# Kernel tuning notes

Hardware: AMD Instinct MI355X
Metric: run time of the kernel (lower is better)

## Reference

```python
import jax, jax.numpy as jnp
import numpy as np

# CCN 'Contract18': the 18 permutation-equivariant ways to reduce a 3rd-order
# vertex-pair tensor T[i,j,k,c] to a 2nd-order tensor out[a,b,c], with
# summations restricted to the neighborhood via the adjacency matrix A.
#  - 6 single-index sums (choose summed index x placement of the two free ones)
#  - 6 diagonal extractions (two indices tied, 3 pairs x 2 placements)
#  - 6 double sums -> vector, broadcast along rows or columns
# Sums over an index m are weighted by A[a, m] (restrict to neighbors of the
# output row node a); diagonal extractions are unweighted.

N = 256
C = 16

def setup_inputs() -> dict:
    key = jax.random.key(0)
    k1, k2 = jax.random.split(key)
    activations = jax.random.normal(k1, (N, N, N, C), dtype=jnp.float32)
    # sparse-ish symmetric binary adjacency, avg degree ~16
    A = (jax.random.uniform(k2, (N, N)) < 16.0 / N).astype(jnp.float32)
    adjacency = jnp.maximum(A, A.T)
    return {"activations": activations, "adjacency": adjacency}

def contract18(T, A):
    # T: (N,N,N,C), A: (N,N)  ->  (N,N,18*C)
    # --- group 1: single-index neighborhood sums (6) ---
    c1 = jnp.einsum('abkc,ak->abc', T, A)
    c2 = jnp.einsum('bakc,ak->abc', T, A)
    c3 = jnp.einsum('ajbc,aj->abc', T, A)
    c4 = jnp.einsum('bjac,aj->abc', T, A)
    c5 = jnp.einsum('iabc,ai->abc', T, A)
    c6 = jnp.einsum('ibac,ai->abc', T, A)
    # --- group 2: diagonal extractions (6) ---
    c7  = jnp.einsum('aabc->abc', T)
    c8  = jnp.einsum('bbac->abc', T)
    c9  = jnp.einsum('abac->abc', T)
    c10 = jnp.einsum('babc->abc', T)
    c11 = jnp.einsum('abbc->abc', T)
    c12 = jnp.einsum('baac->abc', T)
    # --- group 3: double sums -> per-node vectors, broadcast (6) ---
    n = T.shape[0]
    v1 = jnp.einsum('ajkc,aj,ak->ac', T, A, A)  # sum last two indices
    v2 = jnp.einsum('iakc,ai,ak->ac', T, A, A)  # sum outer two indices
    v3 = jnp.einsum('ijac,ai,aj->ac', T, A, A)  # sum first two indices
    ones_row = lambda v: jnp.broadcast_to(v[:, None, :], (n, n, v.shape[-1]))
    ones_col = lambda v: jnp.broadcast_to(v[None, :, :], (n, n, v.shape[-1]))
    c13, c14 = ones_row(v1), ones_col(v1)
    c15, c16 = ones_row(v2), ones_col(v2)
    c17, c18 = ones_row(v3), ones_col(v3)
    return jnp.concatenate([c1, c2, c3, c4, c5, c6, c7, c8, c9, c10, c11, c12,
                            c13, c14, c15, c16, c17, c18], axis=-1)

def reference(activations, adjacency):
    return contract18(activations, adjacency)
```

## Files before the change

### kernel.cpp

```cpp
#include <hip/hip_runtime.h>

#define NN 256
#define CC 16
#define NC (NN*CC)
#define OC (18*CC)

__device__ __forceinline__ void add4(float4& a, const float4 b) {
    a.x += b.x; a.y += b.y; a.z += b.z; a.w += b.w;
}
__device__ __forceinline__ void mad4(float4& a, const float4 b, float m) {
    a.x += b.x*m; a.y += b.y*m; a.z += b.z*m; a.w += b.w*m;
}

__global__ void k_build_nbr(const float* __restrict__ A, short* __restrict__ nbr,
                            int* __restrict__ deg) {
    int a = blockIdx.x;
    int t = threadIdx.x;
    int lane = t & 63, wave = t >> 6;
    bool pred = A[a*NN + t] != 0.0f;
    unsigned long long m = __ballot(pred);
    __shared__ int wcnt[4];
    if (lane == 0) wcnt[wave] = __popcll(m);
    __syncthreads();
    int off = 0;
    for (int w = 0; w < wave; ++w) off += wcnt[w];
    if (pred) {
        int pos = off + __popcll(m & ((1ull << lane) - 1ull));
        nbr[a*NN + pos] = (short)t;
    }
    if (t == 0) deg[a] = wcnt[0] + wcnt[1] + wcnt[2] + wcnt[3];
}

__global__ __launch_bounds__(256) void k_fused(const float4* __restrict__ T4,
                                               const float* __restrict__ A,
                                               const short* __restrict__ nbr,
                                               const int* __restrict__ deg,
                                               float4* __restrict__ out4,
                                               float* __restrict__ vpart) {
    int a = blockIdx.x >> 2;
    int q = blockIdx.x & 3;
    int t = threadIdx.x;
    int v = t & 3, bl = t >> 2;
    int b = q*64 + bl;
    int d = deg[a];

    __shared__ short nbs[NN];
    __shared__ float red[3][64][16];
    for (int e = t; e < d; e += 256) nbs[e] = nbr[a*NN + e];
    __syncthreads();

    const int rowAB = (a*NN + b) << 10;
    const int rowBA = (b*NN + a) << 10;
    const int slabA = a << 18;
    const int slabB = b << 18;
    const int offB  = (b << 2) + v;
    const int offA  = (a << 2) + v;

    float4 z = make_float4(0.f,0.f,0.f,0.f);
    float4 acc1=z, acc2=z, acc3=z, acc4=z, acc5=z, acc6=z;
    #pragma unroll 2
    for (int e = 0; e < d; ++e) {
        int k = nbs[e];
        float4 x1 = T4[rowAB + (k<<2) + v];
        float4 x2 = T4[rowBA + (k<<2) + v];
        float4 x3 = T4[slabA + (k<<10) + offB];
        float4 x4 = T4[slabB + (k<<10) + offA];
        float4 x5 = T4[(k<<18) + (a<<10) + offB];
        float4 x6 = T4[(k<<18) + (b<<10) + offA];
        add4(acc1,x1); add4(acc2,x2); add4(acc3,x3);
        add4(acc4,x4); add4(acc5,x5); add4(acc6,x6);
    }

    float4 d7  = T4[slabA + (a<<10) + offB];
    float4 d8  = T4[slabB + (b<<10) + offA];
    float4 d9  = T4[rowAB + offA];
    float4 d10 = T4[rowBA + offB];
    float4 d11 = T4[rowAB + offB];
    float4 d12 = T4[rowBA + offA];

    const int ob = (a*NN + b)*72;
    out4[ob + 0*4 + v] = acc1;
    out4[ob + 1*4 + v] = acc2;
    out4[ob + 2*4 + v] = acc3;
    out4[ob + 3*4 + v] = acc4;
    out4[ob + 4*4 + v] = acc5;
    out4[ob + 5*4 + v] = acc6;
    out4[ob + 6*4 + v] = d7;
    out4[ob + 7*4 + v] = d8;
    out4[ob + 8*4 + v] = d9;
    out4[ob + 9*4 + v] = d10;
    out4[ob +10*4 + v] = d11;
    out4[ob +11*4 + v] = d12;

    float m = (A[a*NN + b] != 0.0f) ? 1.0f : 0.0f;
    float4 m1=z, m2=z, m3=z;
    mad4(m1, acc1, m); mad4(m2, acc2, m); mad4(m3, acc6, m);
    red[0][bl][v*4+0]=m1.x; red[0][bl][v*4+1]=m1.y; red[0][bl][v*4+2]=m1.z; red[0][bl][v*4+3]=m1.w;
    red[1][bl][v*4+0]=m2.x; red[1][bl][v*4+1]=m2.y; red[1][bl][v*4+2]=m2.z; red[1][bl][v*4+3]=m2.w;
    red[2][bl][v*4+0]=m3.x; red[2][bl][v*4+1]=m3.y; red[2][bl][v*4+2]=m3.z; red[2][bl][v*4+3]=m3.w;
    __syncthreads();
    if (t < 48) {
        int vi = t >> 4, cc = t & 15;
        float s = 0.f;
        for (int i = 0; i < 64; ++i) s += red[vi][i][cc];
        vpart[((a*4 + q)*3 + vi)*CC + cc] = s;
    }
}

__global__ void k_vred(const float* __restrict__ vpart, float* __restrict__ vbuf) {
    int idx = blockIdx.x*256 + threadIdx.x;
    int vi = idx >> 12, rem = idx & 4095;
    int a = rem >> 4, cc = rem & 15;
    float s = 0.f;
    for (int q = 0; q < 4; ++q) s += vpart[((a*4 + q)*3 + vi)*CC + cc];
    vbuf[(vi*NN + a)*CC + cc] = s;
}

__global__ __launch_bounds__(256) void k_broadcast(const float4* __restrict__ vb4,
                                                   float4* __restrict__ out4) {
    int a = blockIdx.x;
    int t = threadIdx.x;
    int v = t & 3, bl = t >> 2;
    float4 v1a = vb4[(0*NN + a)*4 + v];
    float4 v2a = vb4[(1*NN + a)*4 + v];
    float4 v3a = vb4[(2*NN + a)*4 + v];
    for (int b = bl; b < NN; b += 64) {
        float4 v1b = vb4[(0*NN + b)*4 + v];
        float4 v2b = vb4[(1*NN + b)*4 + v];
        float4 v3b = vb4[(2*NN + b)*4 + v];
        int ob = (a*NN + b)*72;
        out4[ob + 48 + v] = v1a;
        out4[ob + 52 + v] = v1b;
        out4[ob + 56 + v] = v2a;
        out4[ob + 60 + v] = v2b;
        out4[ob + 64 + v] = v3a;
        out4[ob + 68 + v] = v3b;
    }
}

extern "C" void kernel_launch(void* const* d_in, const int* in_sizes, int n_in,
                              void* d_out, int out_size, void* d_ws, size_t ws_size,
                              hipStream_t stream) {
    const float* T = (const float*)d_in[0];
    const float* A = (const float*)d_in[1];
    float* out = (float*)d_out;

    char* w = (char*)d_ws;
    short* nbr  = (short*)w;                          w += NN*NN*sizeof(short);
    int*   deg  = (int*)w;                            w += NN*sizeof(int);
    float* vpart= (float*)w;                          w += NN*4*3*CC*sizeof(float);
    float* vbuf = (float*)w;

    hipLaunchKernelGGL(k_build_nbr, dim3(NN),   dim3(NN),  0, stream, A, nbr, deg);
    hipLaunchKernelGGL(k_fused,     dim3(NN*4), dim3(256), 0, stream,
                       (const float4*)T, A, nbr, deg, (float4*)out, vpart);
    hipLaunchKernelGGL(k_vred,      dim3(48),   dim3(256), 0, stream, vpart, vbuf);
    hipLaunchKernelGGL(k_broadcast, dim3(NN),   dim3(256), 0, stream,
                       (const float4*)vbuf, (float4*)out);
}
```

Baseline: 233.6 us.

## Split contraction into per-slab row kernel with LDS atomics and column gather kernel

Replaces the single fused gather kernel with a slab kernel. Each block owns one first index i and walks its rows T[i,j,:,:]. For neighbor rows it reads the whole row; otherwise it reads only the union of the two neighbor lists. From these reads it produces c1, c2 and two diagonals, and it accumulates c3 and c4 through shared-memory atomics. A separate column kernel gathers c5, c6 and the remaining diagonals. The double-sum vectors are now computed by re-reading the written output, replacing the old partial-reduction pass. The aim is to share each row read across several contractions, at the cost of extra full-row reads and atomic contention in shared memory.

```diff
diff --git a/kernel.cpp b/kernel.cpp
--- a/kernel.cpp
+++ b/kernel.cpp
@@ -2,25 +2,26 @@
 
 #define NN 256
 #define CC 16
-#define NC (NN*CC)
-#define OC (18*CC)
+#define OC 288
+
+typedef unsigned long long u64;
 
 __device__ __forceinline__ void add4(float4& a, const float4 b) {
     a.x += b.x; a.y += b.y; a.z += b.z; a.w += b.w;
 }
-__device__ __forceinline__ void mad4(float4& a, const float4 b, float m) {
-    a.x += b.x*m; a.y += b.y*m; a.z += b.z*m; a.w += b.w*m;
+__device__ __forceinline__ void ds_acc4(float* p, const float4 x) {
+    atomicAdd(p+0, x.x); atomicAdd(p+1, x.y); atomicAdd(p+2, x.z); atomicAdd(p+3, x.w);
 }
 
 __global__ void k_build_nbr(const float* __restrict__ A, short* __restrict__ nbr,
-                            int* __restrict__ deg) {
+                            int* __restrict__ deg, u64* __restrict__ umask) {
     int a = blockIdx.x;
     int t = threadIdx.x;
     int lane = t & 63, wave = t >> 6;
     bool pred = A[a*NN + t] != 0.0f;
-    unsigned long long m = __ballot(pred);
+    u64 m = __ballot(pred);
     __shared__ int wcnt[4];
-    if (lane == 0) wcnt[wave] = __popcll(m);
+    if (lane == 0) { wcnt[wave] = __popcll(m); umask[a*4 + wave] = m; }
     __syncthreads();
     int off = 0;
     for (int w = 0; w < wave; ++w) off += wcnt[w];
@@ -31,89 +32,173 @@
     if (t == 0) deg[a] = wcnt[0] + wcnt[1] + wcnt[2] + wcnt[3];
 }
 
-__global__ __launch_bounds__(256) void k_fused(const float4* __restrict__ T4,
-                                               const float* __restrict__ A,
-                                               const short* __restrict__ nbr,
-                                               const int* __restrict__ deg,
-                                               float4* __restrict__ out4,
-                                               float* __restrict__ vpart) {
+__global__ __launch_bounds__(512) void k_slab(const float4* __restrict__ T4,
+                                              const u64* __restrict__ umask,
+                                              float4* __restrict__ out4) {
+    int i = blockIdx.x;
+    int t = threadIdx.x;
+    int wave = t >> 6, lane = t & 63;
+    int g = lane >> 2, v = lane & 3;
+
+    __shared__ u64 masks[NN][4];
+    __shared__ float c3a[NN*19];
+    __shared__ float c4a[NN*19];
+    __shared__ short lists[8][256];
+
+    for (int idx = t; idx < NN*4; idx += 512) ((u64*)masks)[idx] = umask[idx];
+    for (int idx = t; idx < NN*19; idx += 512) { c3a[idx] = 0.f; c4a[idx] = 0.f; }
+    __syncthreads();
+
+    const u64 mi0 = masks[i][0], mi1 = masks[i][1], mi2 = masks[i][2], mi3 = masks[i][3];
+
+    for (int j = wave; j < NN; j += 8) {
+        const float4* row = T4 + ((size_t)(i*NN + j) << 10);
+        u64 mj0 = masks[j][0], mj1 = masks[j][1], mj2 = masks[j][2], mj3 = masks[j][3];
+        u64 miw[4] = {mi0, mi1, mi2, mi3};
+        u64 mjw[4] = {mj0, mj1, mj2, mj3};
+        bool typeA = (miw[j >> 6] >> (j & 63)) & 1;
+        float4 a1 = {0,0,0,0}, a2 = {0,0,0,0};
+
+        if (typeA) {
+            #pragma unroll
+            for (int base = 0; base < NN; base += 32) {
+                const int wq = base >> 6, sh = base & 63;
+                int k0 = base + g, k1 = base + 16 + g;
+                float4 x0 = row[(k0 << 2) + v];
+                float4 x1 = row[(k1 << 2) + v];
+                int b0 = sh + g;
+                bool m1a = (miw[wq] >> b0) & 1, m1b = (miw[wq] >> (b0+16)) & 1;
+                bool m2a = (mjw[wq] >> b0) & 1, m2b = (mjw[wq] >> (b0+16)) & 1;
+                if (m1a) add4(a1, x0);
+                if (m1b) add4(a1, x1);
+                if (m2a) { add4(a2, x0); ds_acc4(&c4a[k0*19 + v*4], x0); }
+                if (m2b) { add4(a2, x1); ds_acc4(&c4a[k1*19 + v*4], x1); }
+                ds_acc4(&c3a[k0*19 + v*4], x0);
+                ds_acc4(&c3a[k1*19 + v*4], x1);
+            }
+        } else {
+            u64 u0 = mi0|mj0, u1 = mi1|mj1, u2 = mi2|mj2, u3 = mi3|mj3;
+            int n0 = __popcll(u0), n1 = __popcll(u1), n2 = __popcll(u2), n3 = __popcll(u3);
+            int n = n0 + n1 + n2 + n3;
+            u64 below = (1ull << lane) - 1ull;
+            if ((u0 >> lane) & 1)
+                lists[wave][__popcll(u0 & below)] =
+                    (short)(lane | (int)((mi0>>lane)&1)<<8 | (int)((mj0>>lane)&1)<<9);
+            if ((u1 >> lane) & 1)
+                lists[wave][n0 + __popcll(u1 & below)] =
+                    (short)((64+lane) | (int)((mi1>>lane)&1)<<8 | (int)((mj1>>lane)&1)<<9);
+            if ((u2 >> lane) & 1)
+                lists[wave][n0+n1 + __popcll(u2 & below)] =
+                    (short)((128+lane) | (int)((mi2>>lane)&1)<<8 | (int)((mj2>>lane)&1)<<9);
+            if ((u3 >> lane) & 1)
+                lists[wave][n0+n1+n2 + __popcll(u3 & below)] =
+                    (short)((192+lane) | (int)((mi3>>lane)&1)<<8 | (int)((mj3>>lane)&1)<<9);
+
+            for (int tt = 0; tt < n; tt += 32) {
+                int e0 = tt + g, e1 = tt + 16 + g;
+                int s0 = (e0 < n) ? (int)lists[wave][e0] : -1;
+                int s1 = (e1 < n) ? (int)lists[wave][e1] : -1;
+                if (s0 >= 0) {
+                    int k = s0 & 255; float4 x = row[(k << 2) + v];
+                    if (s0 & 256) add4(a1, x);
+                    if (s0 & 512) { add4(a2, x); ds_acc4(&c4a[k*19 + v*4], x); }
+                }
+                if (s1 >= 0) {
+                    int k = s1 & 255; float4 x = row[(k << 2) + v];
+                    if (s1 & 256) add4(a1, x);
+                    if (s1 & 512) { add4(a2, x); ds_acc4(&c4a[k*19 + v*4], x); }
+                }
+            }
+        }
+
+        size_t orow = (size_t)(i*NN + j) * 72;
+        if (g == 0) out4[orow + 32 + v] = row[(i << 2) + v];
+        if (g == 1) out4[orow + 40 + v] = row[(j << 2) + v];
+
+        for (int off = 4; off < 64; off <<= 1) {
+            a1.x += __shfl_xor(a1.x, off); a1.y += __shfl_xor(a1.y, off);
+            a1.z += __shfl_xor(a1.z, off); a1.w += __shfl_xor(a1.w, off);
+            a2.x += __shfl_xor(a2.x, off); a2.y += __shfl_xor(a2.y, off);
+            a2.z += __shfl_xor(a2.z, off); a2.w += __shfl_xor(a2.w, off);
+        }
+        if (g == 0) {
+            out4[orow + 0 + v] = a1;
+            out4[(size_t)(j*NN + i) * 72 + 4 + v] = a2;
+        }
+    }
+
+    __syncthreads();
+    for (int idx = t; idx < NN*4; idx += 512) {
+        int k = idx >> 2, q = idx & 3;
+        float4 x3 = {c3a[k*19+q*4+0], c3a[k*19+q*4+1], c3a[k*19+q*4+2], c3a[k*19+q*4+3]};
+        float4 x4 = {c4a[k*19+q*4+0], c4a[k*19+q*4+1], c4a[k*19+q*4+2], c4a[k*19+q*4+3]};
+        out4[(size_t)(i*NN + k)*72 + 8  + q] = x3;
+        out4[(size_t)(k*NN + i)*72 + 12 + q] = x4;
+    }
+}
+
+__global__ __launch_bounds__(256) void k_col(const float4* __restrict__ T4,
+                                             const short* __restrict__ nbr,
+                                             const int* __restrict__ deg,
+                                             float4* __restrict__ out4) {
     int a = blockIdx.x >> 2;
-    int q = blockIdx.x & 3;
-    int t = threadIdx.x;
-    int v = t & 3, bl = t >> 2;
-    int b = q*64 + bl;
+    int qq = blockIdx.x & 3;
+    int t = threadIdx.x;
+    int g = t >> 2, v = t & 3;
     int d = deg[a];
-
     __shared__ short nbs[NN];
-    __shared__ float red[3][64][16];
     for (int e = t; e < d; e += 256) nbs[e] = nbr[a*NN + e];
     __syncthreads();
 
-    const int rowAB = (a*NN + b) << 10;
-    const int rowBA = (b*NN + a) << 10;
-    const int slabA = a << 18;
-    const int slabB = b << 18;
-    const int offB  = (b << 2) + v;
-    const int offA  = (a << 2) + v;
-
-    float4 z = make_float4(0.f,0.f,0.f,0.f);
-    float4 acc1=z, acc2=z, acc3=z, acc4=z, acc5=z, acc6=z;
+    const int b = qq*64 + g;
+    const int qslot = qq*256 + t;
+    float4 a5 = {0,0,0,0};
+    float4 a6 = {0,0,0,0};
     #pragma unroll 2
     for (int e = 0; e < d; ++e) {
-        int k = nbs[e];
-        float4 x1 = T4[rowAB + (k<<2) + v];
-        float4 x2 = T4[rowBA + (k<<2) + v];
-        float4 x3 = T4[slabA + (k<<10) + offB];
-        float4 x4 = T4[slabB + (k<<10) + offA];
-        float4 x5 = T4[(k<<18) + (a<<10) + offB];
-        float4 x6 = T4[(k<<18) + (b<<10) + offA];
-        add4(acc1,x1); add4(acc2,x2); add4(acc3,x3);
-        add4(acc4,x4); add4(acc5,x5); add4(acc6,x6);
-    }
-
-    float4 d7  = T4[slabA + (a<<10) + offB];
-    float4 d8  = T4[slabB + (b<<10) + offA];
-    float4 d9  = T4[rowAB + offA];
-    float4 d10 = T4[rowBA + offB];
-    float4 d11 = T4[rowAB + offB];
-    float4 d12 = T4[rowBA + offA];
-
-    const int ob = (a*NN + b)*72;
-    out4[ob + 0*4 + v] = acc1;
-    out4[ob + 1*4 + v] = acc2;
-    out4[ob + 2*4 + v] = acc3;
-    out4[ob + 3*4 + v] = acc4;
-    out4[ob + 4*4 + v] = acc5;
-    out4[ob + 5*4 + v] = acc6;
-    out4[ob + 6*4 + v] = d7;
-    out4[ob + 7*4 + v] = d8;
-    out4[ob + 8*4 + v] = d9;
-    out4[ob + 9*4 + v] = d10;
-    out4[ob +10*4 + v] = d11;
-    out4[ob +11*4 + v] = d12;
-
-    float m = (A[a*NN + b] != 0.0f) ? 1.0f : 0.0f;
-    float4 m1=z, m2=z, m3=z;
-    mad4(m1, acc1, m); mad4(m2, acc2, m); mad4(m3, acc6, m);
-    red[0][bl][v*4+0]=m1.x; red[0][bl][v*4+1]=m1.y; red[0][bl][v*4+2]=m1.z; red[0][bl][v*4+3]=m1.w;
-    red[1][bl][v*4+0]=m2.x; red[1][bl][v*4+1]=m2.y; red[1][bl][v*4+2]=m2.z; red[1][bl][v*4+3]=m2.w;
-    red[2][bl][v*4+0]=m3.x; red[2][bl][v*4+1]=m3.y; red[2][bl][v*4+2]=m3.z; red[2][bl][v*4+3]=m3.w;
+        int i = nbs[e];
+        float4 x5 = T4[((size_t)(i*NN + a) << 10) + qslot];
+        float4 x6 = T4[((size_t)i << 18) + (b << 10) + (a << 2) + v];
+        add4(a5, x5); add4(a6, x6);
+    }
+    float4 d7  = T4[((size_t)(a*NN + a) << 10) + qslot];
+    float4 d8  = T4[((size_t)(b*NN + b) << 10) + (a << 2) + v];
+    float4 d10 = T4[((size_t)(b*NN + a) << 10) + (b << 2) + v];
+    float4 d12 = T4[((size_t)(b*NN + a) << 10) + (a << 2) + v];
+
+    size_t o = (size_t)(a*NN + b) * 72;
+    out4[o + 16 + v] = a5;
+    out4[o + 20 + v] = a6;
+    out4[o + 24 + v] = d7;
+    out4[o + 28 + v] = d8;
+    out4[o + 36 + v] = d10;
+    out4[o + 44 + v] = d12;
+}
+
+__global__ void k_vsum(const float* __restrict__ out_ro,
+                       const short* __restrict__ nbr, const int* __restrict__ deg,
+                       float* __restrict__ vbuf) {
+    int a = blockIdx.x;
+    int t = threadIdx.x;
+    int c = t & 15, p = t >> 4;
+    int d = deg[a];
+    float s1 = 0.f, s2 = 0.f, s3 = 0.f;
+    for (int e = p; e < d; e += 16) {
+        int b = nbr[a*NN + e];
+        size_t o = (size_t)(a*NN + b) * OC;
+        s1 += out_ro[o + 0  + c];
+        s2 += out_ro[o + 16 + c];
+        s3 += out_ro[o + 80 + c];
+    }
+    __shared__ float red[3][16][17];
+    red[0][p][c] = s1; red[1][p][c] = s2; red[2][p][c] = s3;
     __syncthreads();
     if (t < 48) {
-        int vi = t >> 4, cc = t & 15;
+        int vv = t >> 4, cc = t & 15;
         float s = 0.f;
-        for (int i = 0; i < 64; ++i) s += red[vi][i][cc];
-        vpart[((a*4 + q)*3 + vi)*CC + cc] = s;
-    }
-}
-
-__global__ void k_vred(const float* __restrict__ vpart, float* __restrict__ vbuf) {
-    int idx = blockIdx.x*256 + threadIdx.x;
-    int vi = idx >> 12, rem = idx & 4095;
-    int a = rem >> 4, cc = rem & 15;
-    float s = 0.f;
-    for (int q = 0; q < 4; ++q) s += vpart[((a*4 + q)*3 + vi)*CC + cc];
-    vbuf[(vi*NN + a)*CC + cc] = s;
+        for (int pp = 0; pp < 16; ++pp) s += red[vv][pp][cc];
+        vbuf[(vv*NN + a)*CC + cc] = s;
+    }
 }
 
 __global__ __launch_bounds__(256) void k_broadcast(const float4* __restrict__ vb4,
@@ -128,7 +213,7 @@
         float4 v1b = vb4[(0*NN + b)*4 + v];
         float4 v2b = vb4[(1*NN + b)*4 + v];
         float4 v3b = vb4[(2*NN + b)*4 + v];
-        int ob = (a*NN + b)*72;
+        size_t ob = (size_t)(a*NN + b) * 72;
         out4[ob + 48 + v] = v1a;
         out4[ob + 52 + v] = v1b;
         out4[ob + 56 + v] = v2a;
@@ -146,15 +231,17 @@
     float* out = (float*)d_out;
 
     char* w = (char*)d_ws;
-    short* nbr  = (short*)w;                          w += NN*NN*sizeof(short);
-    int*   deg  = (int*)w;                            w += NN*sizeof(int);
-    float* vpart= (float*)w;                          w += NN*4*3*CC*sizeof(float);
-    float* vbuf = (float*)w;
-
-    hipLaunchKernelGGL(k_build_nbr, dim3(NN),   dim3(NN),  0, stream, A, nbr, deg);
-    hipLaunchKernelGGL(k_fused,     dim3(NN*4), dim3(256), 0, stream,
-                       (const float4*)T, A, nbr, deg, (float4*)out, vpart);
-    hipLaunchKernelGGL(k_vred,      dim3(48),   dim3(256), 0, stream, vpart, vbuf);
+    u64*   umask = (u64*)w;                   w += NN*4*sizeof(u64);
+    short* nbr   = (short*)w;                 w += NN*NN*sizeof(short);
+    int*   deg   = (int*)w;                   w += NN*sizeof(int);
+    float* vbuf  = (float*)w;
+
+    hipLaunchKernelGGL(k_build_nbr, dim3(NN),   dim3(NN),  0, stream, A, nbr, deg, umask);
+    hipLaunchKernelGGL(k_slab,      dim3(NN),   dim3(512), 0, stream,
+                       (const float4*)T, umask, (float4*)out);
+    hipLaunchKernelGGL(k_col,       dim3(NN*4), dim3(256), 0, stream,
+                       (const float4*)T, nbr, deg, (float4*)out);
+    hipLaunchKernelGGL(k_vsum,      dim3(NN),   dim3(256), 0, stream, out, nbr, deg, vbuf);
     hipLaunchKernelGGL(k_broadcast, dim3(NN),   dim3(256), 0, stream,
                        (const float4*)vbuf, (float4*)out);
 }
```

Measured after the change: 533.2 us. 2.28x slower.
